# Optimization experiments

Hardware: AMD Instinct MI355X
Metric: run time of the kernel (lower is better)

The kernel has to match this reference:

```python
import jax, jax.numpy as jnp
import numpy as np

K = 1024   # number of shooting particles (batch_y0.shape[0])
D = 512    # feature dim (batch_y0.shape[2])
M = 4096   # minibatch size of `inp`
T = 6      # number of time points in batch_t
NSUB = 1   # fixed RK4 substeps per interval (replaces adaptive odeint)


def setup_inputs() -> dict:
    key = jax.random.key(0)
    k1, k2, k3 = jax.random.split(key, 3)
    # learned parameters of ShootingBlock (p_params is zeros at init; use small
    # random values so theta/bias are nontrivial for correctness testing)
    x_params = jax.random.normal(k1, (K, 1, D), dtype=jnp.float32)
    p_params = 0.1 * jax.random.normal(k2, (K, 1, D), dtype=jnp.float32)
    Mbar = jnp.eye(D, dtype=jnp.float32)
    Mbar_b = jnp.eye(D, dtype=jnp.float32)
    inp = jax.random.normal(k3, (M, 1, D), dtype=jnp.float32)
    batch_t = jnp.linspace(0.0, 1.0, T).astype(jnp.float32)
    return {"x_params": x_params, "p_params": p_params, "Mbar": Mbar,
            "Mbar_b": Mbar_b, "inp": inp, "batch_t": batch_t}


def _forward(x_params, p_params, Mbar, Mbar_b, inp, batch_t):
    Kp = x_params.shape[0]
    xs = x_params[:, 0, :]                      # [K, d]
    ps = p_params[:, 0, :]                      # [K, d]
    # theta = Mbar^{-1} @ (-p^T @ relu(x))      -> [d, d]
    theta = jnp.linalg.inv(Mbar) @ (-(ps.T) @ jax.nn.relu(xs))
    # bias = Mbar_b^{-1} @ (-p^T @ ones(K,1))   -> [d]
    bias = (jnp.linalg.inv(Mbar_b) @ (-(ps.T) @ jnp.ones((Kp, 1), xs.dtype)))[:, 0]

    def rhs(y):
        # y: [2K + M, d] joint state (x particles, p adjoints, rolled-out input)
        x = y[:Kp]
        p = y[Kp:2 * Kp]
        u = y[2 * Kp:]
        # odefunc_x: dx = theta @ relu(x)^T + bias, transposed back
        dx = jax.nn.relu(x) @ theta.T + bias
        # odefunc_p: dp_i = -diag(x_i >= 0) @ theta^T @ p_i  ==  -(x>=0) * (p @ theta)
        dp = -(x >= 0).astype(y.dtype) * (p @ theta)
        du = jax.nn.relu(u) @ theta.T + bias
        return jnp.concatenate([dx, dp, du], axis=0)

    def rk4(y, dt):
        k1 = rhs(y)
        k2 = rhs(y + 0.5 * dt * k1)
        k3 = rhs(y + 0.5 * dt * k2)
        k4 = rhs(y + dt * k3)
        return y + (dt / 6.0) * (k1 + 2.0 * k2 + 2.0 * k3 + k4)

    y0 = jnp.concatenate([xs, ps, inp[:, 0, :]], axis=0)  # [2K+M, d]

    def step(y, ts):
        t0, t1 = ts
        dt = (t1 - t0) / NSUB
        y = jax.lax.fori_loop(0, NSUB, lambda i, yy: rk4(yy, dt), y)
        return y, y[2 * Kp:]  # emit only the rolled-out input trajectory

    _, traj = jax.lax.scan(step, y0, (batch_t[:-1], batch_t[1:]))
    out = jnp.concatenate([inp[:, 0, :][None], traj], axis=0)  # [T, M, d]
    return out[:, :, None, :]                                   # [T, M, 1, d]


def reference(x_params, p_params, Mbar, Mbar_b, inp, batch_t):
    return _forward(x_params, p_params, Mbar, Mbar_b, inp, batch_t)
```

## Files before the change

### kernel.cpp

```cpp
#include <hip/hip_runtime.h>


namespace {

constexpr int KP = 1024;
constexpr int D  = 512;
constexpr int M  = 4096;

typedef __attribute__((ext_vector_type(8))) short short8;
typedef __attribute__((ext_vector_type(4))) float f32x4;

__device__ __forceinline__ unsigned short f2bf(float f) {
  unsigned int u = __float_as_uint(f);
  u += 0x7FFF + ((u >> 16) & 1);
  return (unsigned short)(u >> 16);
}
__device__ __forceinline__ float bf2f(unsigned short h) {
  return __uint_as_float(((unsigned int)h) << 16);
}

__device__ __forceinline__ void glds16(const unsigned short* g, unsigned short* l) {
  __builtin_amdgcn_global_load_lds(
      (__attribute__((address_space(1))) const void*)g,
      (__attribute__((address_space(3))) void*)l, 16, 0, 0);
}

constexpr int KSPLIT = 8;

__global__ __launch_bounds__(256) void theta_partial_kernel(
    const float* __restrict__ xs, const float* __restrict__ ps,
    float* __restrict__ part) {
  __shared__ float As[32][68];
  __shared__ float Bs[32][68];
  const int d0 = blockIdx.x * 64;
  const int e0 = blockIdx.y * 64;
  const int kb = blockIdx.z * (KP / KSPLIT);
  const int t  = threadIdx.x;
  const int tx = t & 15, ty = t >> 4;
  float acc[4][4] = {};

  for (int k0 = kb; k0 < kb + KP / KSPLIT; k0 += 32) {
#pragma unroll
    for (int p = 0; p < 2; ++p) {
      const int idx = t + p * 256;
      const int c4  = idx & 15;
      const int row = idx >> 4;
      const float4 av = *(const float4*)(ps + (size_t)(k0 + row) * D + d0 + c4 * 4);
      *(float4*)&As[row][c4 * 4] = av;
      float4 bv = *(const float4*)(xs + (size_t)(k0 + row) * D + e0 + c4 * 4);
      bv.x = fmaxf(bv.x, 0.f); bv.y = fmaxf(bv.y, 0.f);
      bv.z = fmaxf(bv.z, 0.f); bv.w = fmaxf(bv.w, 0.f);
      *(float4*)&Bs[row][c4 * 4] = bv;
    }
    __syncthreads();
#pragma unroll
    for (int kk = 0; kk < 32; ++kk) {
      const float4 a4 = *(const float4*)&As[kk][ty * 4];
      const float4 b4 = *(const float4*)&Bs[kk][tx * 4];
      const float a[4] = {a4.x, a4.y, a4.z, a4.w};
      const float b[4] = {b4.x, b4.y, b4.z, b4.w};
#pragma unroll
      for (int i = 0; i < 4; ++i)
#pragma unroll
        for (int j = 0; j < 4; ++j)
          acc[i][j] = fmaf(a[i], b[j], acc[i][j]);
    }
    __syncthreads();
  }
  float* dst = part + (size_t)blockIdx.z * D * D;
#pragma unroll
  for (int i = 0; i < 4; ++i) {
    float4 v;
    v.x = acc[i][0]; v.y = acc[i][1]; v.z = acc[i][2]; v.w = acc[i][3];
    *(float4*)(dst + (size_t)(d0 + ty * 4 + i) * D + e0 + tx * 4) = v;
  }
}

__global__ __launch_bounds__(256) void theta_combine_kernel(
    const float* __restrict__ part, unsigned short* __restrict__ th0,
    unsigned short* __restrict__ th1, unsigned short* __restrict__ th2) {
  const size_t i = (size_t)blockIdx.x * 256 + threadIdx.x;
  float4 s = ((const float4*)part)[i];
#pragma unroll
  for (int z = 1; z < KSPLIT; ++z) {
    const float4 v = ((const float4*)(part + (size_t)z * D * D))[i];
    s.x += v.x; s.y += v.y; s.z += v.z; s.w += v.w;
  }
  const float vv[4] = {-s.x, -s.y, -s.z, -s.w};
  ushort4 h0, h1, h2;
  unsigned short* p0[4] = {&h0.x, &h0.y, &h0.z, &h0.w};
  unsigned short* p1[4] = {&h1.x, &h1.y, &h1.z, &h1.w};
  unsigned short* p2[4] = {&h2.x, &h2.y, &h2.z, &h2.w};
#pragma unroll
  for (int c = 0; c < 4; ++c) {
    const float v = vv[c];
    const unsigned short a0 = f2bf(v);
    const float r1 = v - bf2f(a0);
    const unsigned short a1 = f2bf(r1);
    const float r2 = r1 - bf2f(a1);
    *p0[c] = a0; *p1[c] = a1; *p2[c] = f2bf(r2);
  }
  ((ushort4*)th0)[i] = h0;
  ((ushort4*)th1)[i] = h1;
  ((ushort4*)th2)[i] = h2;
}

__global__ __launch_bounds__(256) void bias_kernel(const float* __restrict__ ps,
                                                   float* __restrict__ bias) {
  __shared__ float part[4][64];
  const int dc = threadIdx.x & 63;
  const int sl = threadIdx.x >> 6;
  const int d  = blockIdx.x * 64 + dc;
  float s = 0.f;
  for (int k = sl * 256; k < sl * 256 + 256; ++k) s += ps[(size_t)k * D + d];
  part[sl][dc] = s;
  __syncthreads();
  if (threadIdx.x < 64) {
    const int c = threadIdx.x;
    bias[blockIdx.x * 64 + c] =
        -(part[0][c] + part[1][c] + part[2][c] + part[3][c]);
  }
}

__global__ __launch_bounds__(256) void init_kernel(
    const float* __restrict__ inp, float* __restrict__ out0,
    unsigned short* __restrict__ y0, unsigned short* __restrict__ y1,
    unsigned short* __restrict__ y2) {
  const size_t i = (size_t)blockIdx.x * 256 + threadIdx.x;
  const float4 v = ((const float4*)inp)[i];
  ((float4*)out0)[i] = v;
  const float vv[4] = {fmaxf(v.x, 0.f), fmaxf(v.y, 0.f),
                       fmaxf(v.z, 0.f), fmaxf(v.w, 0.f)};
  ushort4 h0, h1, h2;
  unsigned short* p0[4] = {&h0.x, &h0.y, &h0.z, &h0.w};
  unsigned short* p1[4] = {&h1.x, &h1.y, &h1.z, &h1.w};
  unsigned short* p2[4] = {&h2.x, &h2.y, &h2.z, &h2.w};
#pragma unroll
  for (int c = 0; c < 4; ++c) {
    const unsigned short a0 = f2bf(vv[c]);
    const float r1 = vv[c] - bf2f(a0);
    const unsigned short a1 = f2bf(r1);
    const float r2 = r1 - bf2f(a1);
    *p0[c] = a0; *p1[c] = a1; *p2[c] = f2bf(r2);
  }
  ((ushort4*)y0)[i] = h0;
  ((ushort4*)y1)[i] = h1;
  ((ushort4*)y2)[i] = h2;
}

template <int MODE>
__global__ __launch_bounds__(256) void feval_kernel(
    const unsigned short* __restrict__ ya0, const unsigned short* __restrict__ ya1,
    const unsigned short* __restrict__ ya2, const unsigned short* __restrict__ th0,
    const unsigned short* __restrict__ th1, const unsigned short* __restrict__ th2,
    const float* __restrict__ bias, const float* __restrict__ bt, int step,
    const float* __restrict__ uStd, float* __restrict__ acc,
    unsigned short* __restrict__ yw0, unsigned short* __restrict__ yw1,
    unsigned short* __restrict__ yw2, float* __restrict__ outStd) {
  __shared__ unsigned short lds[2][2][3][64][32];
  const int t    = threadIdx.x;
  const int w    = t >> 6;
  const int lane = t & 63;
  const int nl   = lane & 15;
  const int qq   = lane >> 4;
  const int m0   = blockIdx.x * 64;
  const int n0   = blockIdx.y * 64;
  const int msb  = (w & 1) * 32;
  const int nsb  = (w >> 1) * 32;
  const float dt = bt[step + 1] - bt[step];
  const unsigned short* Aarr[3] = {ya0, ya1, ya2};
  const unsigned short* Tarr[3] = {th0, th1, th2};

  auto dma = [&](int buf, int slab) {
    const int e0 = slab * 32;
#pragma unroll
    for (int j = 0; j < 3; ++j) {
      const int cb  = (w * 3 + j) * 64;
      const int s   = cb >> 8;
      const int rem = (cb & 255) + lane;
      const int r   = rem >> 2;
      const int q   = (rem & 3) ^ (r & 3);
      unsigned short* dA = &lds[buf][0][0][0][0] + (size_t)cb * 8;
      unsigned short* dB = &lds[buf][1][0][0][0] + (size_t)cb * 8;
      glds16(Aarr[s] + (size_t)(m0 + r) * D + e0 + q * 8, dA);
      glds16(Tarr[s] + (size_t)(n0 + r) * D + e0 + q * 8, dB);
    }
  };

  f32x4 C[2][2];
#pragma unroll
  for (int ms = 0; ms < 2; ++ms)
#pragma unroll
    for (int ns = 0; ns < 2; ++ns) C[ms][ns] = (f32x4){0.f, 0.f, 0.f, 0.f};

  dma(0, 0);
  __syncthreads();

  for (int slab = 0; slab < 16; ++slab) {
    const int buf = slab & 1;
    if (slab + 1 < 16) dma(buf ^ 1, slab + 1);
    short8 av[2][3], bv[2][3];
#pragma unroll
    for (int ms = 0; ms < 2; ++ms) {
      const int r   = msb + ms * 16 + nl;
      const int pos = (qq ^ (r & 3)) * 8;
#pragma unroll
      for (int s = 0; s < 3; ++s)
        av[ms][s] = *(const short8*)&lds[buf][0][s][r][pos];
    }
#pragma unroll
    for (int ns = 0; ns < 2; ++ns) {
      const int r   = nsb + ns * 16 + nl;
      const int pos = (qq ^ (r & 3)) * 8;
#pragma unroll
      for (int s = 0; s < 3; ++s)
        bv[ns][s] = *(const short8*)&lds[buf][1][s][r][pos];
    }
#pragma unroll
    for (int ms = 0; ms < 2; ++ms)
#pragma unroll
      for (int ns = 0; ns < 2; ++ns) {
        f32x4 c = C[ms][ns];
        c = __builtin_amdgcn_mfma_f32_16x16x32_bf16(av[ms][0], bv[ns][0], c, 0, 0, 0);
        c = __builtin_amdgcn_mfma_f32_16x16x32_bf16(av[ms][0], bv[ns][1], c, 0, 0, 0);
        c = __builtin_amdgcn_mfma_f32_16x16x32_bf16(av[ms][1], bv[ns][0], c, 0, 0, 0);
        c = __builtin_amdgcn_mfma_f32_16x16x32_bf16(av[ms][0], bv[ns][2], c, 0, 0, 0);
        c = __builtin_amdgcn_mfma_f32_16x16x32_bf16(av[ms][1], bv[ns][1], c, 0, 0, 0);
        c = __builtin_amdgcn_mfma_f32_16x16x32_bf16(av[ms][2], bv[ns][0], c, 0, 0, 0);
        C[ms][ns] = c;
      }
    __syncthreads();
  }

  const float cn = (MODE == 2) ? dt : 0.5f * dt;
  const float s6 = dt * (1.f / 6.f);
#pragma unroll
  for (int ms = 0; ms < 2; ++ms) {
#pragma unroll
    for (int ns = 0; ns < 2; ++ns) {
      const int n = n0 + nsb + ns * 16 + nl;
      const float bb = bias[n];
#pragma unroll
      for (int r = 0; r < 4; ++r) {
        const int m = m0 + msb + ms * 16 + qq * 4 + r;
        const size_t off = (size_t)m * D + n;
        const float kv = C[ms][ns][r] + bb;
        float y;
        if constexpr (MODE == 0) {
          acc[off] = kv;
          y = fmaf(cn, kv, uStd[off]);
        } else if constexpr (MODE <= 2) {
          const float a = acc[off];
          acc[off] = fmaf(2.f, kv, a);
          y = fmaf(cn, kv, uStd[off]);
        } else {
          const float a = acc[off];
          y = fmaf(s6, a + kv, uStd[off]);
          outStd[off] = y;
        }
        const float ry = fmaxf(y, 0.f);
        const unsigned short h0 = f2bf(ry);
        const float r1 = ry - bf2f(h0);
        const unsigned short h1 = f2bf(r1);
        const float r2 = r1 - bf2f(h1);
        yw0[off] = h0;
        yw1[off] = h1;
        yw2[off] = f2bf(r2);
      }
    }
  }
}

}

extern "C" void kernel_launch(void* const* d_in, const int* in_sizes, int n_in,
                              void* d_out, int out_size, void* d_ws, size_t ws_size,
                              hipStream_t stream) {
  (void)in_sizes; (void)n_in; (void)out_size; (void)ws_size;
  const float* xs  = (const float*)d_in[0];
  const float* ps  = (const float*)d_in[1];
  const float* inp = (const float*)d_in[4];
  const float* bt  = (const float*)d_in[5];
  float* out = (float*)d_out;
  float* ws  = (float*)d_ws;

  float* acc  = ws;
  float* bias = acc + (size_t)M * D;
  unsigned short* th0 = (unsigned short*)(bias + 512);
  unsigned short* th1 = th0 + (size_t)D * D;
  unsigned short* th2 = th1 + (size_t)D * D;
  unsigned short* ya0 = th2 + (size_t)D * D;
  unsigned short* ya1 = ya0 + (size_t)M * D;
  unsigned short* ya2 = ya1 + (size_t)M * D;
  unsigned short* yb0 = ya2 + (size_t)M * D;
  unsigned short* yb1 = yb0 + (size_t)M * D;
  unsigned short* yb2 = yb1 + (size_t)M * D;
  float* part = acc;

  theta_partial_kernel<<<dim3(8, 8, KSPLIT), 256, 0, stream>>>(xs, ps, part);
  theta_combine_kernel<<<(D * D) / (4 * 256), 256, 0, stream>>>(part, th0, th1, th2);
  bias_kernel<<<D / 64, 256, 0, stream>>>(ps, bias);
  init_kernel<<<(M * D) / (4 * 256), 256, 0, stream>>>(inp, out, ya0, ya1, ya2);

  const dim3 grid(M / 64, D / 64);
  for (int s = 0; s < 5; ++s) {
    float* u     = out + (size_t)s * M * D;
    float* unext = out + (size_t)(s + 1) * M * D;
    feval_kernel<0><<<grid, 256, 0, stream>>>(ya0, ya1, ya2, th0, th1, th2, bias,
                                              bt, s, u, acc, yb0, yb1, yb2, nullptr);
    feval_kernel<1><<<grid, 256, 0, stream>>>(yb0, yb1, yb2, th0, th1, th2, bias,
                                              bt, s, u, acc, ya0, ya1, ya2, nullptr);
    feval_kernel<2><<<grid, 256, 0, stream>>>(ya0, ya1, ya2, th0, th1, th2, bias,
                                              bt, s, u, acc, yb0, yb1, yb2, nullptr);
    feval_kernel<3><<<grid, 256, 0, stream>>>(yb0, yb1, yb2, th0, th1, th2, bias,
                                              bt, s, u, acc, ya0, ya1, ya2, unext);
  }
}
```

Before: 589.8 us.

## Use single-wave 64x64 tiles with triple-buffered async LDS loads and no barriers

The RK4 feval GEMM kernel now runs one 64-lane wave per 64x64 output tile instead of four waves. Each wave holds a 4x4 grid of MFMA accumulators. Global-to-LDS loads are triple-buffered two slabs ahead and ordered with explicit vmcnt waits instead of __syncthreads, and the slab loop is fully unrolled. The aim is to remove block-level barriers and raise per-wave MFMA density and LDS operand reuse. The cost is fewer waves per CU for latency hiding, more registers per thread, and a dropped LDS swizzle, which may cause bank conflicts.

```diff
diff --git a/kernel.cpp b/kernel.cpp
--- a/kernel.cpp
+++ b/kernel.cpp
@@ -149,7 +149,7 @@
 }
 
 template <int MODE>
-__global__ __launch_bounds__(256) void feval_kernel(
+__global__ __launch_bounds__(64) void feval_kernel(
     const unsigned short* __restrict__ ya0, const unsigned short* __restrict__ ya1,
     const unsigned short* __restrict__ ya2, const unsigned short* __restrict__ th0,
     const unsigned short* __restrict__ th1, const unsigned short* __restrict__ th2,
@@ -157,94 +157,102 @@
     const float* __restrict__ uStd, float* __restrict__ acc,
     unsigned short* __restrict__ yw0, unsigned short* __restrict__ yw1,
     unsigned short* __restrict__ yw2, float* __restrict__ outStd) {
-  __shared__ unsigned short lds[2][2][3][64][32];
-  const int t    = threadIdx.x;
-  const int w    = t >> 6;
-  const int lane = t & 63;
+  __shared__ unsigned short lds[3][24][512];
+  const int lane = threadIdx.x;
   const int nl   = lane & 15;
   const int qq   = lane >> 4;
   const int m0   = blockIdx.x * 64;
   const int n0   = blockIdx.y * 64;
-  const int msb  = (w & 1) * 32;
-  const int nsb  = (w >> 1) * 32;
   const float dt = bt[step + 1] - bt[step];
-  const unsigned short* Aarr[3] = {ya0, ya1, ya2};
-  const unsigned short* Tarr[3] = {th0, th1, th2};
+
+  float bb[4];
+#pragma unroll
+  for (int ns = 0; ns < 4; ++ns) bb[ns] = bias[n0 + ns * 16 + nl];
+
+  const unsigned short* P[6];
+  P[0] = ya0 + (size_t)(m0 + nl) * D + qq * 8;
+  P[1] = ya1 + (size_t)(m0 + nl) * D + qq * 8;
+  P[2] = ya2 + (size_t)(m0 + nl) * D + qq * 8;
+  P[3] = th0 + (size_t)(n0 + nl) * D + qq * 8;
+  P[4] = th1 + (size_t)(n0 + nl) * D + qq * 8;
+  P[5] = th2 + (size_t)(n0 + nl) * D + qq * 8;
 
   auto dma = [&](int buf, int slab) {
     const int e0 = slab * 32;
 #pragma unroll
-    for (int j = 0; j < 3; ++j) {
-      const int cb  = (w * 3 + j) * 64;
-      const int s   = cb >> 8;
-      const int rem = (cb & 255) + lane;
-      const int r   = rem >> 2;
-      const int q   = (rem & 3) ^ (r & 3);
-      unsigned short* dA = &lds[buf][0][0][0][0] + (size_t)cb * 8;
-      unsigned short* dB = &lds[buf][1][0][0][0] + (size_t)cb * 8;
-      glds16(Aarr[s] + (size_t)(m0 + r) * D + e0 + q * 8, dA);
-      glds16(Tarr[s] + (size_t)(n0 + r) * D + e0 + q * 8, dB);
+    for (int c = 0; c < 24; ++c) {
+      const int ps = c >> 2;
+      const int rg = c & 3;
+      glds16(P[ps] + (size_t)rg * 16 * D + e0, &lds[buf][c][0]);
     }
   };
 
-  f32x4 C[2][2];
-#pragma unroll
-  for (int ms = 0; ms < 2; ++ms)
-#pragma unroll
-    for (int ns = 0; ns < 2; ++ns) C[ms][ns] = (f32x4){0.f, 0.f, 0.f, 0.f};
-
+  f32x4 C[4][4];
+#pragma unroll
+  for (int ms = 0; ms < 4; ++ms)
+#pragma unroll
+    for (int ns = 0; ns < 4; ++ns) C[ms][ns] = (f32x4){0.f, 0.f, 0.f, 0.f};
+
+  asm volatile("s_waitcnt vmcnt(0)" ::: "memory");
   dma(0, 0);
-  __syncthreads();
-
+  dma(1, 1);
+
+#pragma unroll
   for (int slab = 0; slab < 16; ++slab) {
-    const int buf = slab & 1;
-    if (slab + 1 < 16) dma(buf ^ 1, slab + 1);
-    short8 av[2][3], bv[2][3];
-#pragma unroll
-    for (int ms = 0; ms < 2; ++ms) {
-      const int r   = msb + ms * 16 + nl;
-      const int pos = (qq ^ (r & 3)) * 8;
+    const int buf = slab % 3;
+    if (slab + 2 < 16) dma((slab + 2) % 3, slab + 2);
+    if (slab < 14) {
+      asm volatile("s_waitcnt vmcnt(48)" ::: "memory");
+    } else if (slab == 14) {
+      asm volatile("s_waitcnt vmcnt(24)" ::: "memory");
+    } else {
+      asm volatile("s_waitcnt vmcnt(0)" ::: "memory");
+    }
+    __builtin_amdgcn_sched_barrier(0);
+
+    short8 av[4][3];
+#pragma unroll
+    for (int g = 0; g < 4; ++g)
 #pragma unroll
       for (int s = 0; s < 3; ++s)
-        av[ms][s] = *(const short8*)&lds[buf][0][s][r][pos];
-    }
-#pragma unroll
-    for (int ns = 0; ns < 2; ++ns) {
-      const int r   = nsb + ns * 16 + nl;
-      const int pos = (qq ^ (r & 3)) * 8;
-#pragma unroll
-      for (int s = 0; s < 3; ++s)
-        bv[ns][s] = *(const short8*)&lds[buf][1][s][r][pos];
-    }
-#pragma unroll
-    for (int ms = 0; ms < 2; ++ms)
-#pragma unroll
-      for (int ns = 0; ns < 2; ++ns) {
-        f32x4 c = C[ms][ns];
-        c = __builtin_amdgcn_mfma_f32_16x16x32_bf16(av[ms][0], bv[ns][0], c, 0, 0, 0);
-        c = __builtin_amdgcn_mfma_f32_16x16x32_bf16(av[ms][0], bv[ns][1], c, 0, 0, 0);
-        c = __builtin_amdgcn_mfma_f32_16x16x32_bf16(av[ms][1], bv[ns][0], c, 0, 0, 0);
-        c = __builtin_amdgcn_mfma_f32_16x16x32_bf16(av[ms][0], bv[ns][2], c, 0, 0, 0);
-        c = __builtin_amdgcn_mfma_f32_16x16x32_bf16(av[ms][1], bv[ns][1], c, 0, 0, 0);
-        c = __builtin_amdgcn_mfma_f32_16x16x32_bf16(av[ms][2], bv[ns][0], c, 0, 0, 0);
-        C[ms][ns] = c;
-      }
-    __syncthreads();
+        av[g][s] = *(const short8*)&lds[buf][s * 4 + g][lane * 8];
+
+#pragma unroll
+    for (int nh = 0; nh < 2; ++nh) {
+      short8 bv[2][3];
+#pragma unroll
+      for (int g = 0; g < 2; ++g)
+#pragma unroll
+        for (int s = 0; s < 3; ++s)
+          bv[g][s] = *(const short8*)&lds[buf][12 + s * 4 + nh * 2 + g][lane * 8];
+#pragma unroll
+      for (int ms = 0; ms < 4; ++ms)
+#pragma unroll
+        for (int g = 0; g < 2; ++g) {
+          f32x4 c = C[ms][nh * 2 + g];
+          c = __builtin_amdgcn_mfma_f32_16x16x32_bf16(av[ms][0], bv[g][0], c, 0, 0, 0);
+          c = __builtin_amdgcn_mfma_f32_16x16x32_bf16(av[ms][0], bv[g][1], c, 0, 0, 0);
+          c = __builtin_amdgcn_mfma_f32_16x16x32_bf16(av[ms][1], bv[g][0], c, 0, 0, 0);
+          c = __builtin_amdgcn_mfma_f32_16x16x32_bf16(av[ms][0], bv[g][2], c, 0, 0, 0);
+          c = __builtin_amdgcn_mfma_f32_16x16x32_bf16(av[ms][1], bv[g][1], c, 0, 0, 0);
+          c = __builtin_amdgcn_mfma_f32_16x16x32_bf16(av[ms][2], bv[g][0], c, 0, 0, 0);
+          C[ms][nh * 2 + g] = c;
+        }
+    }
   }
 
   const float cn = (MODE == 2) ? dt : 0.5f * dt;
   const float s6 = dt * (1.f / 6.f);
 #pragma unroll
-  for (int ms = 0; ms < 2; ++ms) {
-#pragma unroll
-    for (int ns = 0; ns < 2; ++ns) {
-      const int n = n0 + nsb + ns * 16 + nl;
-      const float bb = bias[n];
+  for (int ms = 0; ms < 4; ++ms) {
+#pragma unroll
+    for (int ns = 0; ns < 4; ++ns) {
+      const int n = n0 + ns * 16 + nl;
 #pragma unroll
       for (int r = 0; r < 4; ++r) {
-        const int m = m0 + msb + ms * 16 + qq * 4 + r;
+        const int m = m0 + ms * 16 + qq * 4 + r;
         const size_t off = (size_t)m * D + n;
-        const float kv = C[ms][ns][r] + bb;
+        const float kv = C[ms][ns][r] + bb[ns];
         float y;
         if constexpr (MODE == 0) {
           acc[off] = kv;
@@ -306,13 +314,13 @@
   for (int s = 0; s < 5; ++s) {
     float* u     = out + (size_t)s * M * D;
     float* unext = out + (size_t)(s + 1) * M * D;
-    feval_kernel<0><<<grid, 256, 0, stream>>>(ya0, ya1, ya2, th0, th1, th2, bias,
-                                              bt, s, u, acc, yb0, yb1, yb2, nullptr);
-    feval_kernel<1><<<grid, 256, 0, stream>>>(yb0, yb1, yb2, th0, th1, th2, bias,
-                                              bt, s, u, acc, ya0, ya1, ya2, nullptr);
-    feval_kernel<2><<<grid, 256, 0, stream>>>(ya0, ya1, ya2, th0, th1, th2, bias,
-                                              bt, s, u, acc, yb0, yb1, yb2, nullptr);
-    feval_kernel<3><<<grid, 256, 0, stream>>>(yb0, yb1, yb2, th0, th1, th2, bias,
-                                              bt, s, u, acc, ya0, ya1, ya2, unext);
-  }
-}
+    feval_kernel<0><<<grid, 64, 0, stream>>>(ya0, ya1, ya2, th0, th1, th2, bias,
+                                             bt, s, u, acc, yb0, yb1, yb2, nullptr);
+    feval_kernel<1><<<grid, 64, 0, stream>>>(yb0, yb1, yb2, th0, th1, th2, bias,
+                                             bt, s, u, acc, ya0, ya1, ya2, nullptr);
+    feval_kernel<2><<<grid, 64, 0, stream>>>(ya0, ya1, ya2, th0, th1, th2, bias,
+                                             bt, s, u, acc, yb0, yb1, yb2, nullptr);
+    feval_kernel<3><<<grid, 64, 0, stream>>>(yb0, yb1, yb2, th0, th1, th2, bias,
+                                             bt, s, u, acc, ya0, ya1, ya2, unext);
+  }
+}
```

Result: slower. 819.0 us (+38.9%).
